# Kernel optimization log

Hardware: AMD Instinct MI355X
Metric: run time of the kernel (lower is better)

The kernel has to match this reference:

```python
import jax, jax.numpy as jnp
import numpy as np

B, K, D = 512, 16, 256
E = 32            # num_experts
H = int(D * 0.25) # d_hidden = 64


def setup_inputs() -> dict:
    key = jax.random.key(0)
    ks = jax.random.split(key, 7)
    d_rs = D ** -0.5
    h_rs = H ** -0.5
    x = jax.random.normal(ks[0], (B, K, D), dtype=jnp.float32)
    router_w = jax.random.uniform(ks[1], (E, D), jnp.float32, -d_rs, d_rs)
    router_b = jax.random.uniform(ks[2], (E,), jnp.float32, -d_rs, d_rs)
    # init_rsqrt_uniform_(weights1, weights1.shape[-1]) -> bound = H**-0.5
    W1 = jax.random.uniform(ks[3], (E, D, H), jnp.float32, -h_rs, h_rs)
    b1 = jax.random.uniform(ks[4], (E, H), jnp.float32, -h_rs, h_rs)
    # init_rsqrt_uniform_(weights2, weights2.shape[-1]) -> bound = D**-0.5
    W2 = jax.random.uniform(ks[5], (E, H, D), jnp.float32, -d_rs, d_rs)
    b2 = jax.random.uniform(ks[6], (E, D), jnp.float32, -d_rs, d_rs)
    return {"x": x, "router_w": router_w, "router_b": router_b,
            "W1": W1, "b1": b1, "W2": W2, "b2": b2}


def reference(x, router_w, router_b, W1, b1, W2, b2):
    # x: [B, K, D] -> flatten tokens: [N, D]
    xf = x.reshape(-1, D)
    logits = xf @ router_w.T + router_b          # [N, E]
    idx = jnp.argmax(logits, axis=-1)            # [N] top-1 expert per token
    # Gather per-token expert weights (honors top-1 sparsity: N*D*H FLOPs,
    # not E*N*D*H dense dispatch).
    w1t = jnp.take(W1, idx, axis=0)              # [N, D, H]
    h = jnp.einsum('nd,ndh->nh', xf, w1t) + jnp.take(b1, idx, axis=0)
    h = jax.nn.relu(h)                           # act1; dropout p=0 is identity
    w2t = jnp.take(W2, idx, axis=0)              # [N, H, D]
    out = jnp.einsum('nh,nhd->nd', h, w2t) + jnp.take(b2, idx, axis=0)
    out = jax.nn.relu(out)                       # original applies act1 again
    return out.reshape(x.shape)
```

## Files before the change

kernel.cpp:

```cpp
#include <hip/hip_runtime.h>
#include <hip/hip_bf16.h>


constexpr int D = 256;
constexpr int H = 64;
constexpr int E = 32;

__global__ __launch_bounds__(256) void moe_top1_kernel(
    const float* __restrict__ x,
    const float* __restrict__ rw,
    const float* __restrict__ rb,
    const float* __restrict__ W1,
    const float* __restrict__ b1,
    const float* __restrict__ W2,
    const float* __restrict__ b2,
    float* __restrict__ out)
{
    __shared__ float xs[D];
    __shared__ float red[8 * E];
    __shared__ float logits[E];
    __shared__ float hred[4][H];
    __shared__ float hs[H];

    const int n = blockIdx.x;
    const int t = threadIdx.x;

    xs[t] = x[n * D + t];
    __syncthreads();

    {
        const int e = t & 31, part = t >> 5;
        const float* w  = rw + e * D + part * 32;
        const float* xp = xs + part * 32;
        float s = 0.f;
#pragma unroll
        for (int k = 0; k < 32; ++k) s += xp[k] * w[k];
        red[part * E + e] = s;
    }
    __syncthreads();
    if (t < E) {
        float s = rb[t];
#pragma unroll
        for (int p = 0; p < 8; ++p) s += red[p * E + t];
        logits[t] = s;
    }
    __syncthreads();

    int eidx;
    {
        float best = logits[0];
        int bi = 0;
#pragma unroll
        for (int i = 1; i < E; ++i) {
            float v = logits[i];
            if (v > best) { best = v; bi = i; }
        }
        eidx = bi;
    }

    {
        const int j = t & 63, p4 = t >> 6;
        const float* w  = W1 + (size_t)eidx * (D * H) + p4 * 64 * H + j;
        const float* xp = xs + p4 * 64;
        float s = 0.f;
#pragma unroll
        for (int k = 0; k < 64; ++k) s += xp[k] * w[k * H];
        hred[p4][j] = s;
    }
    __syncthreads();
    if (t < H) {
        float s = b1[eidx * H + t];
#pragma unroll
        for (int p = 0; p < 4; ++p) s += hred[p][t];
        hs[t] = fmaxf(s, 0.f);
    }
    __syncthreads();

    {
        const float* w = W2 + (size_t)eidx * (H * D) + t;
        float s = b2[eidx * D + t];
#pragma unroll
        for (int k = 0; k < H; ++k) s += hs[k] * w[k * D];
        out[n * D + t] = fmaxf(s, 0.f);
    }
}

extern "C" void kernel_launch(void* const* d_in, const int* in_sizes, int n_in,
                              void* d_out, int out_size, void* d_ws, size_t ws_size,
                              hipStream_t stream) {
    const float* x  = (const float*)d_in[0];
    const float* rw = (const float*)d_in[1];
    const float* rb = (const float*)d_in[2];
    const float* W1 = (const float*)d_in[3];
    const float* b1 = (const float*)d_in[4];
    const float* W2 = (const float*)d_in[5];
    const float* b2 = (const float*)d_in[6];
    float* out = (float*)d_out;

    const int N = in_sizes[0] / D;

    moe_top1_kernel<<<N, 256, 0, stream>>>(x, rw, rb, W1, b1, W2, b2, out);
}
```

Before: 136.6 us.

## Group tokens by expert and tile FFN per expert for weight reuse

Replaces the per-token fused kernel with a pipeline: a batched router kernel computes argmax for 32 tokens per block, a scan builds per-expert offsets and tile lists, a scatter builds a token permutation, and an FFN kernel processes up to 64 same-expert tokens per block. Each block reads the expert weights once per tile through uniform (scalar) addresses instead of once per token, removing most of the redundant W1/W2 traffic. It adds four launches plus a memset and relies on atomics. MAX_TILES of 160 caps the tile count, and the per-expert tile rounding must fit under that cap.

```diff
diff --git a/kernel.cpp b/kernel.cpp
--- a/kernel.cpp
+++ b/kernel.cpp
@@ -5,83 +5,203 @@
 constexpr int D = 256;
 constexpr int H = 64;
 constexpr int E = 32;
-
-__global__ __launch_bounds__(256) void moe_top1_kernel(
+constexpr int TPB_R = 32;
+constexpr int T_TILE = 64;
+constexpr int MAX_TILES = 160;
+
+__global__ __launch_bounds__(256) void router_kernel(
+    const float* __restrict__ x, const float* __restrict__ rw,
+    const float* __restrict__ rb, int* __restrict__ ws)
+{
+    __shared__ float4 xs[TPB_R][66];
+    __shared__ float4 rws[E][66];
+    __shared__ float logitS[TPB_R][E + 1];
+
+    const int t = threadIdx.x;
+    const int n0 = blockIdx.x * TPB_R;
+
+    const float4* x4 = (const float4*)x;
+    const float4* rw4 = (const float4*)rw;
+    for (int i = t; i < TPB_R * 64; i += 256) {
+        int r = i >> 6, q = i & 63;
+        xs[r][q] = x4[(size_t)(n0 + r) * 64 + q];
+        rws[r][q] = rw4[r * 64 + q];
+    }
+    __syncthreads();
+
+    const int e = t & 31;
+    const int g = t >> 3 >> 2;
+    float s[4];
+#pragma unroll
+    for (int j = 0; j < 4; ++j) s[j] = rb[e];
+#pragma unroll
+    for (int p = 0; p < 8; ++p) {
+        float sp[4] = {0.f, 0.f, 0.f, 0.f};
+#pragma unroll
+        for (int k4 = 0; k4 < 8; ++k4) {
+            float4 wv = rws[e][p * 8 + k4];
+#pragma unroll
+            for (int j = 0; j < 4; ++j) {
+                float4 xv = xs[g * 4 + j][p * 8 + k4];
+                sp[j] = fmaf(xv.x, wv.x, sp[j]);
+                sp[j] = fmaf(xv.y, wv.y, sp[j]);
+                sp[j] = fmaf(xv.z, wv.z, sp[j]);
+                sp[j] = fmaf(xv.w, wv.w, sp[j]);
+            }
+        }
+#pragma unroll
+        for (int j = 0; j < 4; ++j) s[j] += sp[j];
+    }
+#pragma unroll
+    for (int j = 0; j < 4; ++j) logitS[g * 4 + j][e] = s[j];
+    __syncthreads();
+
+    if (t < TPB_R) {
+        float best = logitS[t][0];
+        int bi = 0;
+#pragma unroll
+        for (int i = 1; i < E; ++i) {
+            float v = logitS[t][i];
+            if (v > best) { best = v; bi = i; }
+        }
+        ws[1024 + n0 + t] = bi;
+        atomicAdd(&ws[bi], 1);
+    }
+}
+
+__global__ void scan_kernel(int* __restrict__ ws)
+{
+    __shared__ int cts[E];
+    __shared__ int offs[E + 1];
+    const int t = threadIdx.x;
+    if (t < E) cts[t] = ws[t];
+    __syncthreads();
+    if (t == 0) {
+        int off = 0;
+        for (int e2 = 0; e2 < E; ++e2) { offs[e2] = off; off += cts[e2]; }
+        offs[E] = off;
+    }
+    __syncthreads();
+    if (t < E) { ws[64 + t] = offs[t]; ws[32 + t] = offs[t]; }
+    if (t == E) ws[64 + E] = offs[E];
+    if (t == 0) {
+        int nt = 0;
+        for (int e2 = 0; e2 < E; ++e2)
+            for (int s2 = 0; s2 < cts[e2]; s2 += T_TILE) {
+                ws[128 + nt] = e2;
+                ws[320 + nt] = offs[e2] + s2;
+                ++nt;
+            }
+        for (; nt < MAX_TILES; ++nt) ws[128 + nt] = -1;
+    }
+}
+
+__global__ __launch_bounds__(256) void scatter_kernel(int* __restrict__ ws)
+{
+    const int n = blockIdx.x * 256 + threadIdx.x;
+    const int e = ws[1024 + n];
+    const int pos = atomicAdd(&ws[32 + e], 1);
+    ws[9216 + pos] = n;
+}
+
+__global__ __launch_bounds__(256) void ffn_kernel(
     const float* __restrict__ x,
-    const float* __restrict__ rw,
-    const float* __restrict__ rb,
-    const float* __restrict__ W1,
-    const float* __restrict__ b1,
-    const float* __restrict__ W2,
-    const float* __restrict__ b2,
-    float* __restrict__ out)
-{
-    __shared__ float xs[D];
-    __shared__ float red[8 * E];
-    __shared__ float logits[E];
-    __shared__ float hred[4][H];
-    __shared__ float hs[H];
-
-    const int n = blockIdx.x;
+    const float* __restrict__ W1, const float* __restrict__ b1,
+    const float* __restrict__ W2, const float* __restrict__ b2,
+    const int* __restrict__ ws, float* __restrict__ out)
+{
+    __shared__ float xsl[T_TILE][260];
+    __shared__ float hsl[T_TILE][68];
+
+    const int b = blockIdx.x;
+    const int e = ws[128 + b];
+    if (e < 0) return;
+    const int start = ws[320 + b];
+    const int cnt = min(T_TILE, ws[64 + e + 1] - start);
     const int t = threadIdx.x;
-
-    xs[t] = x[n * D + t];
-    __syncthreads();
+    const int lane = t & 63;
+    const int w = t >> 6;
+    const int* __restrict__ perm = ws + 9216;
 
     {
-        const int e = t & 31, part = t >> 5;
-        const float* w  = rw + e * D + part * 32;
-        const float* xp = xs + part * 32;
-        float s = 0.f;
-#pragma unroll
-        for (int k = 0; k < 32; ++k) s += xp[k] * w[k];
-        red[part * E + e] = s;
-    }
-    __syncthreads();
-    if (t < E) {
-        float s = rb[t];
-#pragma unroll
-        for (int p = 0; p < 8; ++p) s += red[p * E + t];
-        logits[t] = s;
-    }
-    __syncthreads();
-
-    int eidx;
-    {
-        float best = logits[0];
-        int bi = 0;
-#pragma unroll
-        for (int i = 1; i < E; ++i) {
-            float v = logits[i];
-            if (v > best) { best = v; bi = i; }
-        }
-        eidx = bi;
-    }
-
-    {
-        const int j = t & 63, p4 = t >> 6;
-        const float* w  = W1 + (size_t)eidx * (D * H) + p4 * 64 * H + j;
-        const float* xp = xs + p4 * 64;
-        float s = 0.f;
-#pragma unroll
-        for (int k = 0; k < 64; ++k) s += xp[k] * w[k * H];
-        hred[p4][j] = s;
-    }
-    __syncthreads();
-    if (t < H) {
-        float s = b1[eidx * H + t];
-#pragma unroll
-        for (int p = 0; p < 4; ++p) s += hred[p][t];
-        hs[t] = fmaxf(s, 0.f);
-    }
-    __syncthreads();
-
-    {
-        const float* w = W2 + (size_t)eidx * (H * D) + t;
-        float s = b2[eidx * D + t];
-#pragma unroll
-        for (int k = 0; k < H; ++k) s += hs[k] * w[k * D];
-        out[n * D + t] = fmaxf(s, 0.f);
+        const float4* x4 = (const float4*)x;
+        for (int i = t; i < cnt * 64; i += 256) {
+            int r = i >> 6, q = i & 63;
+            int row = perm[start + r];
+            *(float4*)&xsl[r][q * 4] = x4[(size_t)row * 64 + q];
+        }
+    }
+    __syncthreads();
+
+    const float* w1e = W1 + (size_t)e * (D * H);
+    const int c0 = __builtin_amdgcn_readfirstlane(w * 16);
+
+    float acc[16];
+#pragma unroll
+    for (int j = 0; j < 16; ++j) acc[j] = b1[e * H + c0 + j];
+    for (int k4 = 0; k4 < 64; ++k4) {
+        float4 xv = *(const float4*)&xsl[lane][k4 * 4];
+        const float* r0 = w1e + (k4 * 4 + 0) * H + c0;
+        const float* r1 = w1e + (k4 * 4 + 1) * H + c0;
+        const float* r2 = w1e + (k4 * 4 + 2) * H + c0;
+        const float* r3 = w1e + (k4 * 4 + 3) * H + c0;
+#pragma unroll
+        for (int j = 0; j < 16; ++j) {
+            acc[j] = fmaf(xv.x, r0[j], acc[j]);
+            acc[j] = fmaf(xv.y, r1[j], acc[j]);
+            acc[j] = fmaf(xv.z, r2[j], acc[j]);
+            acc[j] = fmaf(xv.w, r3[j], acc[j]);
+        }
+    }
+#pragma unroll
+    for (int j4 = 0; j4 < 4; ++j4) {
+        float4 v;
+        v.x = fmaxf(acc[j4 * 4 + 0], 0.f);
+        v.y = fmaxf(acc[j4 * 4 + 1], 0.f);
+        v.z = fmaxf(acc[j4 * 4 + 2], 0.f);
+        v.w = fmaxf(acc[j4 * 4 + 3], 0.f);
+        *(float4*)&hsl[lane][c0 + j4 * 4] = v;
+    }
+    __syncthreads();
+
+    const float* w2e = W2 + (size_t)e * (H * D);
+    const int d0 = __builtin_amdgcn_readfirstlane(w * 64);
+
+    float acc2[64];
+#pragma unroll
+    for (int j = 0; j < 64; ++j) acc2[j] = b2[e * D + d0 + j];
+#pragma unroll
+    for (int jc = 0; jc < 4; ++jc) {
+        float* a = acc2 + jc * 16;
+        const float* wbase = w2e + d0 + jc * 16;
+        for (int k4 = 0; k4 < 16; ++k4) {
+            float4 hv = *(const float4*)&hsl[lane][k4 * 4];
+            const float* r0 = wbase + (k4 * 4 + 0) * D;
+            const float* r1 = wbase + (k4 * 4 + 1) * D;
+            const float* r2 = wbase + (k4 * 4 + 2) * D;
+            const float* r3 = wbase + (k4 * 4 + 3) * D;
+#pragma unroll
+            for (int j = 0; j < 16; ++j) {
+                a[j] = fmaf(hv.x, r0[j], a[j]);
+                a[j] = fmaf(hv.y, r1[j], a[j]);
+                a[j] = fmaf(hv.z, r2[j], a[j]);
+                a[j] = fmaf(hv.w, r3[j], a[j]);
+            }
+        }
+    }
+
+    if (lane < cnt) {
+        const int row = perm[start + lane];
+        float4* o4 = (float4*)out;
+#pragma unroll
+        for (int j4 = 0; j4 < 16; ++j4) {
+            float4 v;
+            v.x = fmaxf(acc2[j4 * 4 + 0], 0.f);
+            v.y = fmaxf(acc2[j4 * 4 + 1], 0.f);
+            v.z = fmaxf(acc2[j4 * 4 + 2], 0.f);
+            v.w = fmaxf(acc2[j4 * 4 + 3], 0.f);
+            o4[(size_t)row * 64 + (d0 >> 2) + j4] = v;
+        }
     }
 }
 
@@ -96,8 +216,13 @@
     const float* W2 = (const float*)d_in[5];
     const float* b2 = (const float*)d_in[6];
     float* out = (float*)d_out;
+    int* ws = (int*)d_ws;
 
     const int N = in_sizes[0] / D;
 
-    moe_top1_kernel<<<N, 256, 0, stream>>>(x, rw, rb, W1, b1, W2, b2, out);
-}
+    hipMemsetAsync(ws, 0, 128, stream);
+    router_kernel<<<N / TPB_R, 256, 0, stream>>>(x, rw, rb, ws);
+    scan_kernel<<<1, 256, 0, stream>>>(ws);
+    scatter_kernel<<<N / 256, 256, 0, stream>>>(ws);
+    ffn_kernel<<<MAX_TILES, 256, 0, stream>>>(x, W1, b1, W2, b2, ws, out);
+}
```

Result: slower. 177.5 us (+29.9%).
